# Kernel tuning notes

Measured on AMD Instinct MI355X. Metric: run time of the kernel, lower is better.

The kernel has to match this reference:

```python
import jax, jax.numpy as jnp
import numpy as np

N_NODES = 50000
N_EDGES = 1600000
D_IN = 48
D_OUT = 48


def setup_inputs() -> dict:
    key = jax.random.key(0)
    k1, k2, k3, k4 = jax.random.split(key, 4)
    features = jax.random.normal(k1, (N_NODES, D_IN), dtype=jnp.float32)
    src = jax.random.randint(k2, (N_EDGES,), 0, N_NODES, dtype=jnp.int64)
    dst = jax.random.randint(k3, (N_EDGES,), 0, N_NODES, dtype=jnp.int64)
    # xavier_normal for Linear(48,48): std = sqrt(2/(fan_in+fan_out))
    std = np.sqrt(2.0 / (D_IN + D_OUT))
    W = jax.random.normal(k4, (D_OUT, D_IN), dtype=jnp.float32) * std
    b = jnp.zeros((D_OUT,), dtype=jnp.float32)
    return {"features": features, "src": src, "dst": dst, "W": W, "b": b}


def reference(features, src, dst, W, b):
    n = features.shape[0]
    ones = jnp.ones(src.shape[0], dtype=features.dtype)
    out_deg = jax.ops.segment_sum(ones, src, num_segments=n)
    in_deg = jax.ops.segment_sum(ones, dst, num_segments=n)
    ci = jax.lax.rsqrt(jnp.maximum(out_deg, 1.0))  # per src node
    cj = jax.lax.rsqrt(jnp.maximum(in_deg, 1.0))   # per dst node
    # gather-scale: m_e = h[src_e] * ci[src_e]
    msg = features[src] * ci[src][:, None]          # [E, D_IN]
    # scatter-sum to dst, then scale by cj
    agg = jax.ops.segment_sum(msg, dst, num_segments=n) * cj[:, None]
    # DGL update_all leaves zero-in-degree nodes with their original 'h'
    h = jnp.where(in_deg[:, None] > 0, agg, features)
    out = jax.nn.relu(h @ W.T + b)
    return out
```

## Files before the change

kernel.cpp:

```cpp
#include <hip/hip_runtime.h>

#define N_NODES 50000
#define N_EDGES 1600000
#define D 48

#define EPB 8192
#define PB  196
#define NPB_D 64
#define NBIN_D 782
#define NPB_S 256
#define NBIN_S 196

#define EMAX 3072
#define HS 52

#define RECD_OFF  0
#define SRCB_OFF  6422528
#define CI_OFF    8028160
#define OFFLD_OFF 8228160
#define OFFLS_OFF 8535096

__global__ __launch_bounds__(1024) void k_prep(const int* __restrict__ src,
                                               const int* __restrict__ dst,
                                               unsigned int* __restrict__ rec,
                                               unsigned char* __restrict__ srcb,
                                               unsigned short* __restrict__ offld,
                                               unsigned short* __restrict__ offls) {
    __shared__ int cd[NBIN_D];
    __shared__ int cs[NBIN_S];
    __shared__ int scan[1024];
    __shared__ alignas(16) unsigned int  bufd[EPB];
    __shared__ alignas(16) unsigned char bufs[EPB];
    int tid = threadIdx.x, p = blockIdx.x;
    int base = p * EPB;

    int sv[8], dv[8];
    bool ok[8];
    #pragma unroll
    for (int k = 0; k < 8; ++k) {
        int e = base + tid + k * 1024;
        ok[k] = (e < N_EDGES);
        sv[k] = ok[k] ? src[e] : 0;
        dv[k] = ok[k] ? dst[e] : 0;
    }

    for (int i = tid; i < NBIN_D; i += 1024) cd[i] = 0;
    for (int i = tid; i < NBIN_S; i += 1024) cs[i] = 0;
    __syncthreads();
    #pragma unroll
    for (int k = 0; k < 8; ++k) {
        if (ok[k]) {
            atomicAdd(&cd[dv[k] >> 6], 1);
            atomicAdd(&cs[sv[k] >> 8], 1);
        }
    }
    __syncthreads();

    int own = 0;
    if (tid < NBIN_D) own = cd[tid];
    else if (tid < NBIN_D + NBIN_S) own = cs[tid - NBIN_D];
    scan[tid] = own;
    __syncthreads();
    for (int o = 1; o < 1024; o <<= 1) {
        int x = (tid >= o) ? scan[tid - o] : 0;
        __syncthreads();
        scan[tid] += x;
        __syncthreads();
    }
    int incl = scan[tid];
    int cdt = scan[NBIN_D - 1];
    __syncthreads();

    if (tid < NBIN_D) {
        int ex = incl - own;
        offld[p * (NBIN_D + 1) + tid] = (unsigned short)ex;
        cd[tid] = ex;
        if (tid == NBIN_D - 1) offld[p * (NBIN_D + 1) + NBIN_D] = (unsigned short)incl;
    } else if (tid < NBIN_D + NBIN_S) {
        int t = tid - NBIN_D;
        int ex = (incl - cdt) - own;
        offls[p * (NBIN_S + 1) + t] = (unsigned short)ex;
        cs[t] = ex;
        if (t == NBIN_S - 1) offls[p * (NBIN_S + 1) + NBIN_S] = (unsigned short)(incl - cdt);
    }
    __syncthreads();

    #pragma unroll
    for (int k = 0; k < 8; ++k) {
        if (ok[k]) {
            int s = sv[k], d = dv[k];
            int pd = atomicAdd(&cd[d >> 6], 1);
            bufd[pd] = ((unsigned int)s << 6) | (unsigned int)(d & 63);
            int ps = atomicAdd(&cs[s >> 8], 1);
            bufs[ps] = (unsigned char)s;
        }
    }
    __syncthreads();

    int4* ro = (int4*)(rec + base);
    const int4* bi = (const int4*)bufd;
    for (int i = tid; i < EPB / 4; i += 1024) ro[i] = bi[i];
    unsigned int* so = (unsigned int*)(srcb + base);
    const unsigned int* bs = (const unsigned int*)bufs;
    for (int i = tid; i < EPB / 4; i += 1024) so[i] = bs[i];
}

__global__ __launch_bounds__(512) void k_ci(const unsigned char* __restrict__ srcb,
                                            const unsigned short* __restrict__ offls,
                                            float* __restrict__ ci) {
    __shared__ int cnt[NPB_S];
    int tid = threadIdx.x, sb = blockIdx.x;
    for (int i = tid; i < NPB_S; i += 512) cnt[i] = 0;
    __syncthreads();
    int wave = tid >> 6, lane = tid & 63;
    for (int p = wave; p < PB; p += 8) {
        int beg = offls[p * (NBIN_S + 1) + sb];
        int end = offls[p * (NBIN_S + 1) + sb + 1];
        for (int j = beg + lane; j < end; j += 64)
            atomicAdd(&cnt[srcb[p * EPB + j]], 1);
    }
    __syncthreads();
    int n = sb * NPB_S + tid;
    if (tid < NPB_S && n < N_NODES)
        ci[n] = rsqrtf(fmaxf((float)cnt[tid], 1.0f));
}

__global__ __launch_bounds__(1024, 8) void k_gcn(
    const unsigned int* __restrict__ rec, const unsigned short* __restrict__ offld,
    const float* __restrict__ ci, const float* __restrict__ feat,
    const float* __restrict__ W, const float* __restrict__ b,
    float* __restrict__ out) {
    __shared__ int   craw[EMAX];
    __shared__ int   colb[EMAX];
    __shared__ float hl[NPB_D * HS];
    __shared__ float Wl[D * HS];
    __shared__ float bl[D];
    __shared__ int   ideg[NPB_D];
    __shared__ int   off[NPB_D];
    __shared__ int   cur[NPB_D];
    __shared__ int   runoff[PB + 1];
    __shared__ int   runpos[PB];
    __shared__ int   rs[256];
    int tid = threadIdx.x, bin = blockIdx.x;

    for (int i = tid; i < D * D; i += 1024) Wl[(i / D) * HS + (i % D)] = W[i];
    if (tid < D) bl[tid] = b[tid];
    if (tid < NPB_D) { ideg[tid] = 0; cur[tid] = 0; }

    int rlen = 0;
    if (tid < PB) {
        int o0 = offld[tid * (NBIN_D + 1) + bin];
        int o1 = offld[tid * (NBIN_D + 1) + bin + 1];
        rlen = o1 - o0;
        runpos[tid] = tid * EPB + o0;
    }
    if (tid < 256) rs[tid] = (tid < PB) ? rlen : 0;
    __syncthreads();
    for (int o = 1; o < 256; o <<= 1) {
        int x = 0;
        if (tid < 256 && tid >= o) x = rs[tid - o];
        __syncthreads();
        if (tid < 256) rs[tid] += x;
        __syncthreads();
    }
    if (tid < PB) runoff[tid] = rs[tid] - rlen;
    if (tid == 0) runoff[PB] = rs[PB - 1];
    __syncthreads();
    int cnt = runoff[PB];
    if (cnt > EMAX) cnt = EMAX;

    for (int j = tid; j < cnt; j += 1024) {
        int lo = 0, hi = PB - 1;
        while (lo < hi) {
            int mid = (lo + hi + 1) >> 1;
            if (runoff[mid] <= j) lo = mid; else hi = mid - 1;
        }
        unsigned int r = rec[runpos[lo] + (j - runoff[lo])];
        craw[j] = (int)r;
        atomicAdd(&ideg[r & 63], 1);
    }
    __syncthreads();
    if (tid < NPB_D) {
        int v = ideg[tid];
        int incl = v;
        for (int o = 1; o < 64; o <<= 1) {
            int u = __shfl_up(incl, o);
            if (tid >= o) incl += u;
        }
        off[tid] = incl - v;
    }
    __syncthreads();
    for (int j = tid; j < cnt; j += 1024) {
        int r = craw[j];
        int dl = r & 63;
        int p = atomicAdd(&cur[dl], 1);
        colb[off[dl] + p] = r >> 6;
    }
    __syncthreads();

    int wave = tid >> 6;
    int lane = tid & 63;
    int eslot = lane / 12;
    int d4 = lane - eslot * 12;
    bool lane_ok = (lane < 60);
    const float4* feat4 = (const float4*)feat;

    for (int q = 0; q < 4; ++q) {
        int nl = wave * 4 + q;
        int n = bin * NPB_D + nl;
        int cb = off[nl];
        int deg = ideg[nl];

        float4 acc = make_float4(0.0f, 0.0f, 0.0f, 0.0f);
        for (int c0 = 0; c0 < deg; c0 += 60) {
            int jn = min(60, deg - c0);
            int colv = (lane < jn) ? colb[cb + c0 + lane] : 0;
            float civ = (lane < jn) ? ci[colv] : 0.0f;
            for (int i = 0; i < jn; i += 5) {
                int ei = i + eslot;
                int s = __shfl(colv, ei);
                float c = __shfl(civ, ei);
                if (lane_ok && ei < jn) {
                    float4 f = feat4[(size_t)s * 12 + d4];
                    acc.x = fmaf(f.x, c, acc.x);
                    acc.y = fmaf(f.y, c, acc.y);
                    acc.z = fmaf(f.z, c, acc.z);
                    acc.w = fmaf(f.w, c, acc.w);
                }
            }
        }
        {
            float x1 = __shfl(acc.x, lane + 12), x2 = __shfl(acc.x, lane + 24);
            float x3 = __shfl(acc.x, lane + 36), x4 = __shfl(acc.x, lane + 48);
            float y1 = __shfl(acc.y, lane + 12), y2 = __shfl(acc.y, lane + 24);
            float y3 = __shfl(acc.y, lane + 36), y4 = __shfl(acc.y, lane + 48);
            float z1 = __shfl(acc.z, lane + 12), z2 = __shfl(acc.z, lane + 24);
            float z3 = __shfl(acc.z, lane + 36), z4 = __shfl(acc.z, lane + 48);
            float w1 = __shfl(acc.w, lane + 12), w2 = __shfl(acc.w, lane + 24);
            float w3 = __shfl(acc.w, lane + 36), w4 = __shfl(acc.w, lane + 48);
            acc.x += (x1 + x2) + (x3 + x4);
            acc.y += (y1 + y2) + (y3 + y4);
            acc.z += (z1 + z2) + (z3 + z4);
            acc.w += (w1 + w2) + (w3 + w4);
        }
        if (lane < 12 && n < N_NODES) {
            float4 res;
            if (deg > 0) {
                float cj = rsqrtf((float)deg);
                res = make_float4(acc.x * cj, acc.y * cj, acc.z * cj, acc.w * cj);
            } else {
                res = feat4[(size_t)n * 12 + d4];
            }
            *(float4*)(hl + nl * HS + d4 * 4) = res;
        }
    }
    __syncthreads();

    {
        int nl = tid >> 4;
        int c = tid & 15;
        int n = bin * NPB_D + nl;
        if (n < N_NODES) {
            float a0 = bl[c], a1 = bl[c + 16], a2 = bl[c + 32];
            #pragma unroll
            for (int k4 = 0; k4 < 12; ++k4) {
                float4 hv = *(const float4*)(hl + nl * HS + k4 * 4);
                float4 w0 = *(const float4*)(Wl + c * HS + k4 * 4);
                float4 w1 = *(const float4*)(Wl + (c + 16) * HS + k4 * 4);
                float4 w2 = *(const float4*)(Wl + (c + 32) * HS + k4 * 4);
                a0 = fmaf(hv.x, w0.x, a0); a0 = fmaf(hv.y, w0.y, a0);
                a0 = fmaf(hv.z, w0.z, a0); a0 = fmaf(hv.w, w0.w, a0);
                a1 = fmaf(hv.x, w1.x, a1); a1 = fmaf(hv.y, w1.y, a1);
                a1 = fmaf(hv.z, w1.z, a1); a1 = fmaf(hv.w, w1.w, a1);
                a2 = fmaf(hv.x, w2.x, a2); a2 = fmaf(hv.y, w2.y, a2);
                a2 = fmaf(hv.z, w2.z, a2); a2 = fmaf(hv.w, w2.w, a2);
            }
            float* op = out + (size_t)n * D;
            op[c]      = fmaxf(a0, 0.0f);
            op[c + 16] = fmaxf(a1, 0.0f);
            op[c + 32] = fmaxf(a2, 0.0f);
        }
    }
}

extern "C" void kernel_launch(void* const* d_in, const int* in_sizes, int n_in,
                              void* d_out, int out_size, void* d_ws, size_t ws_size,
                              hipStream_t stream) {
    const float* feat = (const float*)d_in[0];
    const int*   src  = (const int*)d_in[1];
    const int*   dst  = (const int*)d_in[2];
    const float* W    = (const float*)d_in[3];
    const float* b    = (const float*)d_in[4];
    float* out = (float*)d_out;

    char* ws = (char*)d_ws;
    unsigned int*   rec   = (unsigned int*)(ws + RECD_OFF);
    unsigned char*  srcb  = (unsigned char*)(ws + SRCB_OFF);
    float*          ci    = (float*)(ws + CI_OFF);
    unsigned short* offld = (unsigned short*)(ws + OFFLD_OFF);
    unsigned short* offls = (unsigned short*)(ws + OFFLS_OFF);

    k_prep<<<PB, 1024, 0, stream>>>(src, dst, rec, srcb, offld, offls);
    k_ci<<<NBIN_S, 512, 0, stream>>>(srcb, offls, ci);
    k_gcn<<<NBIN_D, 1024, 0, stream>>>(rec, offld, ci, feat, W, b, out);
}
```

Baseline: 159.5 us.

## Fuse three GCN kernels into one persistent kernel with grid barriers

```diff
diff --git a/kernel.cpp b/kernel.cpp
--- a/kernel.cpp
+++ b/kernel.cpp
@@ -4,8 +4,9 @@
 #define N_EDGES 1600000
 #define D 48
 
-#define EPB 8192
-#define PB  196
+#define NB  256
+#define TPB 1024
+#define EPB 6272
 #define NPB_D 64
 #define NBIN_D 782
 #define NPB_S 256
@@ -18,267 +19,315 @@
 #define SRCB_OFF  6422528
 #define CI_OFF    8028160
 #define OFFLD_OFF 8228160
-#define OFFLS_OFF 8535096
-
-__global__ __launch_bounds__(1024) void k_prep(const int* __restrict__ src,
-                                               const int* __restrict__ dst,
-                                               unsigned int* __restrict__ rec,
-                                               unsigned char* __restrict__ srcb,
-                                               unsigned short* __restrict__ offld,
-                                               unsigned short* __restrict__ offls) {
-    __shared__ int cd[NBIN_D];
-    __shared__ int cs[NBIN_S];
-    __shared__ int scan[1024];
-    __shared__ alignas(16) unsigned int  bufd[EPB];
-    __shared__ alignas(16) unsigned char bufs[EPB];
-    int tid = threadIdx.x, p = blockIdx.x;
-    int base = p * EPB;
-
-    int sv[8], dv[8];
-    bool ok[8];
-    #pragma unroll
-    for (int k = 0; k < 8; ++k) {
-        int e = base + tid + k * 1024;
-        ok[k] = (e < N_EDGES);
-        sv[k] = ok[k] ? src[e] : 0;
-        dv[k] = ok[k] ? dst[e] : 0;
-    }
-
-    for (int i = tid; i < NBIN_D; i += 1024) cd[i] = 0;
-    for (int i = tid; i < NBIN_S; i += 1024) cs[i] = 0;
+#define OFFLS_OFF 8629056
+#define BAR_OFF   8729920
+
+__device__ __forceinline__ void gridbar(int* bar, int target) {
     __syncthreads();
-    #pragma unroll
-    for (int k = 0; k < 8; ++k) {
-        if (ok[k]) {
-            atomicAdd(&cd[dv[k] >> 6], 1);
-            atomicAdd(&cs[sv[k] >> 8], 1);
-        }
+    if (threadIdx.x == 0) {
+        __threadfence();
+        atomicAdd(bar, 1);
+        while (atomicAdd(bar, 0) < target)
+            __builtin_amdgcn_s_sleep(4);
+        __threadfence();
     }
     __syncthreads();
-
-    int own = 0;
-    if (tid < NBIN_D) own = cd[tid];
-    else if (tid < NBIN_D + NBIN_S) own = cs[tid - NBIN_D];
-    scan[tid] = own;
-    __syncthreads();
-    for (int o = 1; o < 1024; o <<= 1) {
-        int x = (tid >= o) ? scan[tid - o] : 0;
-        __syncthreads();
-        scan[tid] += x;
-        __syncthreads();
+}
+
+__global__ __launch_bounds__(TPB) void k_fused(
+    const int* __restrict__ src, const int* __restrict__ dst,
+    const float* __restrict__ feat, const float* __restrict__ W,
+    const float* __restrict__ b, float* __restrict__ out,
+    unsigned int* __restrict__ rec, unsigned char* __restrict__ srcb,
+    float* __restrict__ ci, unsigned short* __restrict__ offld,
+    unsigned short* __restrict__ offls, int* bar) {
+
+    __shared__ union U_t {
+        struct {
+            unsigned int bufd[EPB];
+            int scan[TPB];
+            int cd[NBIN_D];
+            int cs[NBIN_S];
+            unsigned char bufs[EPB];
+        } p1;
+        struct { int cnt[NPB_S]; } p2;
+        struct {
+            int   craw[EMAX];
+            int   colb[EMAX];
+            float hl[NPB_D * HS];
+            float Wl[D * HS];
+            float bl[D];
+            int   ideg[NPB_D];
+            int   off[NPB_D];
+            int   cur[NPB_D];
+            int   runpos[NB];
+            int   runoff[NB + 1];
+            int   rs[NB];
+        } p3;
+    } U;
+    static_assert(sizeof(U.p1) < 160 * 1024 && sizeof(U.p3) < 160 * 1024, "lds");
+
+    int tid = threadIdx.x, blk = blockIdx.x;
+
+    {
+        int base = blk * EPB;
+        int sv[7], dv[7];
+        bool ok[7];
+        #pragma unroll
+        for (int k = 0; k < 7; ++k) {
+            int j = tid + k * TPB;
+            int e = base + j;
+            ok[k] = (j < EPB) && (e < N_EDGES);
+            sv[k] = ok[k] ? src[e] : 0;
+            dv[k] = ok[k] ? dst[e] : 0;
+        }
+        for (int i = tid; i < NBIN_D; i += TPB) U.p1.cd[i] = 0;
+        for (int i = tid; i < NBIN_S; i += TPB) U.p1.cs[i] = 0;
+        __syncthreads();
+        #pragma unroll
+        for (int k = 0; k < 7; ++k) {
+            if (ok[k]) {
+                atomicAdd(&U.p1.cd[dv[k] >> 6], 1);
+                atomicAdd(&U.p1.cs[sv[k] >> 8], 1);
+            }
+        }
+        __syncthreads();
+
+        int own = 0;
+        if (tid < NBIN_D) own = U.p1.cd[tid];
+        else if (tid < NBIN_D + NBIN_S) own = U.p1.cs[tid - NBIN_D];
+        U.p1.scan[tid] = own;
+        __syncthreads();
+        for (int o = 1; o < TPB; o <<= 1) {
+            int x = (tid >= o) ? U.p1.scan[tid - o] : 0;
+            __syncthreads();
+            U.p1.scan[tid] += x;
+            __syncthreads();
+        }
+        int incl = U.p1.scan[tid];
+        int cdt = U.p1.scan[NBIN_D - 1];
+        __syncthreads();
+
+        if (tid < NBIN_D) {
+            int ex = incl - own;
+            offld[blk * (NBIN_D + 1) + tid] = (unsigned short)ex;
+            U.p1.cd[tid] = ex;
+            if (tid == NBIN_D - 1) offld[blk * (NBIN_D + 1) + NBIN_D] = (unsigned short)incl;
+        } else if (tid < NBIN_D + NBIN_S) {
+            int t = tid - NBIN_D;
+            int ex = (incl - cdt) - own;
+            offls[blk * (NBIN_S + 1) + t] = (unsigned short)ex;
+            U.p1.cs[t] = ex;
+            if (t == NBIN_S - 1) offls[blk * (NBIN_S + 1) + NBIN_S] = (unsigned short)(incl - cdt);
+        }
+        __syncthreads();
+
+        #pragma unroll
+        for (int k = 0; k < 7; ++k) {
+            if (ok[k]) {
+                int s = sv[k], d = dv[k];
+                int pd = atomicAdd(&U.p1.cd[d >> 6], 1);
+                U.p1.bufd[pd] = ((unsigned int)s << 6) | (unsigned int)(d & 63);
+                int ps = atomicAdd(&U.p1.cs[s >> 8], 1);
+                U.p1.bufs[ps] = (unsigned char)s;
+            }
+        }
+        __syncthreads();
+
+        int4* ro = (int4*)(rec + base);
+        const int4* bi = (const int4*)U.p1.bufd;
+        for (int i = tid; i < EPB / 4; i += TPB) ro[i] = bi[i];
+        unsigned int* so = (unsigned int*)(srcb + base);
+        const unsigned int* bs = (const unsigned int*)U.p1.bufs;
+        for (int i = tid; i < EPB / 4; i += TPB) so[i] = bs[i];
     }
-    int incl = scan[tid];
-    int cdt = scan[NBIN_D - 1];
-    __syncthreads();
-
-    if (tid < NBIN_D) {
-        int ex = incl - own;
-        offld[p * (NBIN_D + 1) + tid] = (unsigned short)ex;
-        cd[tid] = ex;
-        if (tid == NBIN_D - 1) offld[p * (NBIN_D + 1) + NBIN_D] = (unsigned short)incl;
-    } else if (tid < NBIN_D + NBIN_S) {
-        int t = tid - NBIN_D;
-        int ex = (incl - cdt) - own;
-        offls[p * (NBIN_S + 1) + t] = (unsigned short)ex;
-        cs[t] = ex;
-        if (t == NBIN_S - 1) offls[p * (NBIN_S + 1) + NBIN_S] = (unsigned short)(incl - cdt);
+
+    gridbar(bar, NB);
+
+    if (blk < NBIN_S) {
+        int sb = blk;
+        if (tid < NPB_S) U.p2.cnt[tid] = 0;
+        __syncthreads();
+        int wave = tid >> 6, lane = tid & 63;
+        for (int p = wave; p < NB; p += 16) {
+            int o0 = offls[p * (NBIN_S + 1) + sb];
+            int o1 = offls[p * (NBIN_S + 1) + sb + 1];
+            for (int j = o0 + lane; j < o1; j += 64)
+                atomicAdd(&U.p2.cnt[srcb[p * EPB + j]], 1);
+        }
+        __syncthreads();
+        if (tid < NPB_S) {
+            int n = sb * NPB_S + tid;
+            if (n < N_NODES) ci[n] = rsqrtf(fmaxf((float)U.p2.cnt[tid], 1.0f));
+        }
     }
-    __syncthreads();
-
-    #pragma unroll
-    for (int k = 0; k < 8; ++k) {
-        if (ok[k]) {
-            int s = sv[k], d = dv[k];
-            int pd = atomicAdd(&cd[d >> 6], 1);
-            bufd[pd] = ((unsigned int)s << 6) | (unsigned int)(d & 63);
-            int ps = atomicAdd(&cs[s >> 8], 1);
-            bufs[ps] = (unsigned char)s;
-        }
-    }
-    __syncthreads();
-
-    int4* ro = (int4*)(rec + base);
-    const int4* bi = (const int4*)bufd;
-    for (int i = tid; i < EPB / 4; i += 1024) ro[i] = bi[i];
-    unsigned int* so = (unsigned int*)(srcb + base);
-    const unsigned int* bs = (const unsigned int*)bufs;
-    for (int i = tid; i < EPB / 4; i += 1024) so[i] = bs[i];
-}
-
-__global__ __launch_bounds__(512) void k_ci(const unsigned char* __restrict__ srcb,
-                                            const unsigned short* __restrict__ offls,
-                                            float* __restrict__ ci) {
-    __shared__ int cnt[NPB_S];
-    int tid = threadIdx.x, sb = blockIdx.x;
-    for (int i = tid; i < NPB_S; i += 512) cnt[i] = 0;
-    __syncthreads();
+
+    gridbar(bar, 2 * NB);
+
+    for (int i = tid; i < D * D; i += TPB) U.p3.Wl[(i / D) * HS + (i % D)] = W[i];
+    if (tid < D) U.p3.bl[tid] = b[tid];
+
     int wave = tid >> 6, lane = tid & 63;
-    for (int p = wave; p < PB; p += 8) {
-        int beg = offls[p * (NBIN_S + 1) + sb];
-        int end = offls[p * (NBIN_S + 1) + sb + 1];
-        for (int j = beg + lane; j < end; j += 64)
-            atomicAdd(&cnt[srcb[p * EPB + j]], 1);
-    }
-    __syncthreads();
-    int n = sb * NPB_S + tid;
-    if (tid < NPB_S && n < N_NODES)
-        ci[n] = rsqrtf(fmaxf((float)cnt[tid], 1.0f));
-}
-
-__global__ __launch_bounds__(1024, 8) void k_gcn(
-    const unsigned int* __restrict__ rec, const unsigned short* __restrict__ offld,
-    const float* __restrict__ ci, const float* __restrict__ feat,
-    const float* __restrict__ W, const float* __restrict__ b,
-    float* __restrict__ out) {
-    __shared__ int   craw[EMAX];
-    __shared__ int   colb[EMAX];
-    __shared__ float hl[NPB_D * HS];
-    __shared__ float Wl[D * HS];
-    __shared__ float bl[D];
-    __shared__ int   ideg[NPB_D];
-    __shared__ int   off[NPB_D];
-    __shared__ int   cur[NPB_D];
-    __shared__ int   runoff[PB + 1];
-    __shared__ int   runpos[PB];
-    __shared__ int   rs[256];
-    int tid = threadIdx.x, bin = blockIdx.x;
-
-    for (int i = tid; i < D * D; i += 1024) Wl[(i / D) * HS + (i % D)] = W[i];
-    if (tid < D) bl[tid] = b[tid];
-    if (tid < NPB_D) { ideg[tid] = 0; cur[tid] = 0; }
-
-    int rlen = 0;
-    if (tid < PB) {
-        int o0 = offld[tid * (NBIN_D + 1) + bin];
-        int o1 = offld[tid * (NBIN_D + 1) + bin + 1];
-        rlen = o1 - o0;
-        runpos[tid] = tid * EPB + o0;
-    }
-    if (tid < 256) rs[tid] = (tid < PB) ? rlen : 0;
-    __syncthreads();
-    for (int o = 1; o < 256; o <<= 1) {
-        int x = 0;
-        if (tid < 256 && tid >= o) x = rs[tid - o];
-        __syncthreads();
-        if (tid < 256) rs[tid] += x;
-        __syncthreads();
-    }
-    if (tid < PB) runoff[tid] = rs[tid] - rlen;
-    if (tid == 0) runoff[PB] = rs[PB - 1];
-    __syncthreads();
-    int cnt = runoff[PB];
-    if (cnt > EMAX) cnt = EMAX;
-
-    for (int j = tid; j < cnt; j += 1024) {
-        int lo = 0, hi = PB - 1;
-        while (lo < hi) {
-            int mid = (lo + hi + 1) >> 1;
-            if (runoff[mid] <= j) lo = mid; else hi = mid - 1;
-        }
-        unsigned int r = rec[runpos[lo] + (j - runoff[lo])];
-        craw[j] = (int)r;
-        atomicAdd(&ideg[r & 63], 1);
-    }
-    __syncthreads();
-    if (tid < NPB_D) {
-        int v = ideg[tid];
-        int incl = v;
-        for (int o = 1; o < 64; o <<= 1) {
-            int u = __shfl_up(incl, o);
-            if (tid >= o) incl += u;
-        }
-        off[tid] = incl - v;
-    }
-    __syncthreads();
-    for (int j = tid; j < cnt; j += 1024) {
-        int r = craw[j];
-        int dl = r & 63;
-        int p = atomicAdd(&cur[dl], 1);
-        colb[off[dl] + p] = r >> 6;
-    }
-    __syncthreads();
-
-    int wave = tid >> 6;
-    int lane = tid & 63;
     int eslot = lane / 12;
     int d4 = lane - eslot * 12;
     bool lane_ok = (lane < 60);
     const float4* feat4 = (const float4*)feat;
 
-    for (int q = 0; q < 4; ++q) {
-        int nl = wave * 4 + q;
-        int n = bin * NPB_D + nl;
-        int cb = off[nl];
-        int deg = ideg[nl];
-
-        float4 acc = make_float4(0.0f, 0.0f, 0.0f, 0.0f);
-        for (int c0 = 0; c0 < deg; c0 += 60) {
-            int jn = min(60, deg - c0);
-            int colv = (lane < jn) ? colb[cb + c0 + lane] : 0;
-            float civ = (lane < jn) ? ci[colv] : 0.0f;
-            for (int i = 0; i < jn; i += 5) {
+    for (int bin = blk; bin < NBIN_D; bin += NB) {
+        __syncthreads();
+        if (tid < NPB_D) { U.p3.ideg[tid] = 0; U.p3.cur[tid] = 0; }
+        int rl = 0;
+        if (tid < NB) {
+            int o0 = offld[tid * (NBIN_D + 1) + bin];
+            int o1 = offld[tid * (NBIN_D + 1) + bin + 1];
+            rl = o1 - o0;
+            U.p3.runpos[tid] = tid * EPB + o0;
+            U.p3.rs[tid] = rl;
+        }
+        __syncthreads();
+        for (int o = 1; o < NB; o <<= 1) {
+            int x = 0;
+            if (tid < NB && tid >= o) x = U.p3.rs[tid - o];
+            __syncthreads();
+            if (tid < NB) U.p3.rs[tid] += x;
+            __syncthreads();
+        }
+        if (tid < NB) U.p3.runoff[tid] = U.p3.rs[tid] - rl;
+        if (tid == 0) U.p3.runoff[NB] = U.p3.rs[NB - 1];
+        __syncthreads();
+
+        {
+            int r = tid >> 2, sub = tid & 3;
+            int rbase = U.p3.runoff[r];
+            int rlen = U.p3.runoff[r + 1] - rbase;
+            int gpos = U.p3.runpos[r];
+            for (int j = sub; j < rlen; j += 4) {
+                int idx = rbase + j;
+                if (idx < EMAX) {
+                    int v = (int)rec[gpos + j];
+                    U.p3.craw[idx] = v;
+                    atomicAdd(&U.p3.ideg[v & 63], 1);
+                }
+            }
+        }
+        __syncthreads();
+        int cnt = U.p3.runoff[NB];
+        if (cnt > EMAX) cnt = EMAX;
+
+        if (tid < NPB_D) {
+            int v = U.p3.ideg[tid];
+            int incl = v;
+            for (int o = 1; o < 64; o <<= 1) {
+                int u = __shfl_up(incl, o);
+                if (tid >= o) incl += u;
+            }
+            U.p3.off[tid] = incl - v;
+        }
+        __syncthreads();
+        for (int j = tid; j < cnt; j += TPB) {
+            int r = U.p3.craw[j];
+            int dl = r & 63;
+            int p = atomicAdd(&U.p3.cur[dl], 1);
+            U.p3.colb[U.p3.off[dl] + p] = r >> 6;
+        }
+        __syncthreads();
+
+        int nl0 = wave * 4;
+        int degq[4], cbq[4];
+        float4 acc[4];
+        #pragma unroll
+        for (int q = 0; q < 4; ++q) {
+            degq[q] = U.p3.ideg[nl0 + q];
+            cbq[q] = U.p3.off[nl0 + q];
+            acc[q] = make_float4(0.0f, 0.0f, 0.0f, 0.0f);
+        }
+        int maxdeg = max(max(degq[0], degq[1]), max(degq[2], degq[3]));
+        for (int c0 = 0; c0 < maxdeg; c0 += 60) {
+            int colv[4]; float civ[4]; int jnq[4];
+            #pragma unroll
+            for (int q = 0; q < 4; ++q) {
+                int jn = degq[q] - c0;
+                jnq[q] = jn < 60 ? jn : 60;
+                colv[q] = (lane < jnq[q]) ? U.p3.colb[cbq[q] + c0 + lane] : 0;
+                civ[q]  = (lane < jnq[q]) ? ci[colv[q]] : 0.0f;
+            }
+            int rem = maxdeg - c0;
+            int maxjn = rem < 60 ? rem : 60;
+            for (int i = 0; i < maxjn; i += 5) {
                 int ei = i + eslot;
-                int s = __shfl(colv, ei);
-                float c = __shfl(civ, ei);
-                if (lane_ok && ei < jn) {
-                    float4 f = feat4[(size_t)s * 12 + d4];
-                    acc.x = fmaf(f.x, c, acc.x);
-                    acc.y = fmaf(f.y, c, acc.y);
-                    acc.z = fmaf(f.z, c, acc.z);
-                    acc.w = fmaf(f.w, c, acc.w);
-                }
-            }
-        }
+                int sq[4]; float cq[4];
+                #pragma unroll
+                for (int q = 0; q < 4; ++q) {
+                    sq[q] = __shfl(colv[q], ei);
+                    cq[q] = __shfl(civ[q], ei);
+                }
+                #pragma unroll
+                for (int q = 0; q < 4; ++q) {
+                    if (lane_ok && ei < jnq[q]) {
+                        float4 f = feat4[(size_t)sq[q] * 12 + d4];
+                        acc[q].x = fmaf(f.x, cq[q], acc[q].x);
+                        acc[q].y = fmaf(f.y, cq[q], acc[q].y);
+                        acc[q].z = fmaf(f.z, cq[q], acc[q].z);
+                        acc[q].w = fmaf(f.w, cq[q], acc[q].w);
+                    }
+                }
+            }
+        }
+        #pragma unroll
+        for (int q = 0; q < 4; ++q) {
+            float4 a = acc[q];
+            float x1 = __shfl(a.x, lane + 12), x2 = __shfl(a.x, lane + 24);
+            float x3 = __shfl(a.x, lane + 36), x4 = __shfl(a.x, lane + 48);
+            float y1 = __shfl(a.y, lane + 12), y2 = __shfl(a.y, lane + 24);
+            float y3 = __shfl(a.y, lane + 36), y4 = __shfl(a.y, lane + 48);
+            float z1 = __shfl(a.z, lane + 12), z2 = __shfl(a.z, lane + 24);
+            float z3 = __shfl(a.z, lane + 36), z4 = __shfl(a.z, lane + 48);
+            float w1 = __shfl(a.w, lane + 12), w2 = __shfl(a.w, lane + 24);
+            float w3 = __shfl(a.w, lane + 36), w4 = __shfl(a.w, lane + 48);
+            a.x += (x1 + x2) + (x3 + x4);
+            a.y += (y1 + y2) + (y3 + y4);
+            a.z += (z1 + z2) + (z3 + z4);
+            a.w += (w1 + w2) + (w3 + w4);
+            int nl = nl0 + q;
+            int n = bin * NPB_D + nl;
+            if (lane < 12 && n < N_NODES) {
+                float4 res;
+                int deg = degq[q];
+                if (deg > 0) {
+                    float cj = rsqrtf((float)deg);
+                    res = make_float4(a.x * cj, a.y * cj, a.z * cj, a.w * cj);
+                } else {
+                    res = feat4[(size_t)n * 12 + d4];
+                }
+                *(float4*)(U.p3.hl + nl * HS + d4 * 4) = res;
+            }
+        }
+        __syncthreads();
+
         {
-            float x1 = __shfl(acc.x, lane + 12), x2 = __shfl(acc.x, lane + 24);
-            float x3 = __shfl(acc.x, lane + 36), x4 = __shfl(acc.x, lane + 48);
-            float y1 = __shfl(acc.y, lane + 12), y2 = __shfl(acc.y, lane + 24);
-            float y3 = __shfl(acc.y, lane + 36), y4 = __shfl(acc.y, lane + 48);
-            float z1 = __shfl(acc.z, lane + 12), z2 = __shfl(acc.z, lane + 24);
-            float z3 = __shfl(acc.z, lane + 36), z4 = __shfl(acc.z, lane + 48);
-            float w1 = __shfl(acc.w, lane + 12), w2 = __shfl(acc.w, lane + 24);
-            float w3 = __shfl(acc.w, lane + 36), w4 = __shfl(acc.w, lane + 48);
-            acc.x += (x1 + x2) + (x3 + x4);
-            acc.y += (y1 + y2) + (y3 + y4);
-            acc.z += (z1 + z2) + (z3 + z4);
-            acc.w += (w1 + w2) + (w3 + w4);
-        }
-        if (lane < 12 && n < N_NODES) {
-            float4 res;
-            if (deg > 0) {
-                float cj = rsqrtf((float)deg);
-                res = make_float4(acc.x * cj, acc.y * cj, acc.z * cj, acc.w * cj);
-            } else {
-                res = feat4[(size_t)n * 12 + d4];
-            }
-            *(float4*)(hl + nl * HS + d4 * 4) = res;
-        }
-    }
-    __syncthreads();
-
-    {
-        int nl = tid >> 4;
-        int c = tid & 15;
-        int n = bin * NPB_D + nl;
-        if (n < N_NODES) {
-            float a0 = bl[c], a1 = bl[c + 16], a2 = bl[c + 32];
-            #pragma unroll
-            for (int k4 = 0; k4 < 12; ++k4) {
-                float4 hv = *(const float4*)(hl + nl * HS + k4 * 4);
-                float4 w0 = *(const float4*)(Wl + c * HS + k4 * 4);
-                float4 w1 = *(const float4*)(Wl + (c + 16) * HS + k4 * 4);
-                float4 w2 = *(const float4*)(Wl + (c + 32) * HS + k4 * 4);
-                a0 = fmaf(hv.x, w0.x, a0); a0 = fmaf(hv.y, w0.y, a0);
-                a0 = fmaf(hv.z, w0.z, a0); a0 = fmaf(hv.w, w0.w, a0);
-                a1 = fmaf(hv.x, w1.x, a1); a1 = fmaf(hv.y, w1.y, a1);
-                a1 = fmaf(hv.z, w1.z, a1); a1 = fmaf(hv.w, w1.w, a1);
-                a2 = fmaf(hv.x, w2.x, a2); a2 = fmaf(hv.y, w2.y, a2);
-                a2 = fmaf(hv.z, w2.z, a2); a2 = fmaf(hv.w, w2.w, a2);
-            }
-            float* op = out + (size_t)n * D;
-            op[c]      = fmaxf(a0, 0.0f);
-            op[c + 16] = fmaxf(a1, 0.0f);
-            op[c + 32] = fmaxf(a2, 0.0f);
+            int nl = tid >> 4;
+            int c = tid & 15;
+            int n = bin * NPB_D + nl;
+            if (n < N_NODES) {
+                float a0 = U.p3.bl[c], a1 = U.p3.bl[c + 16], a2 = U.p3.bl[c + 32];
+                #pragma unroll
+                for (int k4 = 0; k4 < 12; ++k4) {
+                    float4 hv = *(const float4*)(U.p3.hl + nl * HS + k4 * 4);
+                    float4 w0 = *(const float4*)(U.p3.Wl + c * HS + k4 * 4);
+                    float4 w1 = *(const float4*)(U.p3.Wl + (c + 16) * HS + k4 * 4);
+                    float4 w2 = *(const float4*)(U.p3.Wl + (c + 32) * HS + k4 * 4);
+                    a0 = fmaf(hv.x, w0.x, a0); a0 = fmaf(hv.y, w0.y, a0);
+                    a0 = fmaf(hv.z, w0.z, a0); a0 = fmaf(hv.w, w0.w, a0);
+                    a1 = fmaf(hv.x, w1.x, a1); a1 = fmaf(hv.y, w1.y, a1);
+                    a1 = fmaf(hv.z, w1.z, a1); a1 = fmaf(hv.w, w1.w, a1);
+                    a2 = fmaf(hv.x, w2.x, a2); a2 = fmaf(hv.y, w2.y, a2);
+                    a2 = fmaf(hv.z, w2.z, a2); a2 = fmaf(hv.w, w2.w, a2);
+                }
+                float* op = out + (size_t)n * D;
+                op[c]      = fmaxf(a0, 0.0f);
+                op[c + 16] = fmaxf(a1, 0.0f);
+                op[c + 32] = fmaxf(a2, 0.0f);
+            }
         }
     }
 }
@@ -299,8 +348,9 @@
     float*          ci    = (float*)(ws + CI_OFF);
     unsigned short* offld = (unsigned short*)(ws + OFFLD_OFF);
     unsigned short* offls = (unsigned short*)(ws + OFFLS_OFF);
-
-    k_prep<<<PB, 1024, 0, stream>>>(src, dst, rec, srcb, offld, offls);
-    k_ci<<<NBIN_S, 512, 0, stream>>>(srcb, offls, ci);
-    k_gcn<<<NBIN_D, 1024, 0, stream>>>(rec, offld, ci, feat, W, b, out);
+    int*            bar   = (int*)(ws + BAR_OFF);
+
+    hipMemsetAsync(bar, 0, 8, stream);
+    k_fused<<<NB, TPB, 0, stream>>>(src, dst, feat, W, b, out,
+                                    rec, srcb, ci, offld, offls, bar);
 }
```

Measured after the change: 237.0 us. 48.6% more time.

## Prescale features by ci in k_ci, use wave-shuffle scans, halve gcn block size

Applied to the files above, without the earlier changes.

```diff
diff --git a/kernel.cpp b/kernel.cpp
--- a/kernel.cpp
+++ b/kernel.cpp
@@ -16,9 +16,11 @@
 
 #define RECD_OFF  0
 #define SRCB_OFF  6422528
-#define CI_OFF    8028160
-#define OFFLD_OFF 8228160
-#define OFFLS_OFF 8535096
+#define OFFLD_OFF 8028160
+#define OFFLS_OFF 8335104
+#define CI_OFF    8412416
+#define SFEAT_OFF 8612416
+#define SFEAT_END 18212416
 
 __global__ __launch_bounds__(1024) void k_prep(const int* __restrict__ src,
                                                const int* __restrict__ dst,
@@ -28,10 +30,12 @@
                                                unsigned short* __restrict__ offls) {
     __shared__ int cd[NBIN_D];
     __shared__ int cs[NBIN_S];
-    __shared__ int scan[1024];
+    __shared__ int wsum[16], wexcl[16];
+    __shared__ int cdt_s;
     __shared__ alignas(16) unsigned int  bufd[EPB];
     __shared__ alignas(16) unsigned char bufs[EPB];
     int tid = threadIdx.x, p = blockIdx.x;
+    int wave = tid >> 6, lane = tid & 63;
     int base = p * EPB;
 
     int sv[8], dv[8];
@@ -59,29 +63,41 @@
     int own = 0;
     if (tid < NBIN_D) own = cd[tid];
     else if (tid < NBIN_D + NBIN_S) own = cs[tid - NBIN_D];
-    scan[tid] = own;
-    __syncthreads();
-    for (int o = 1; o < 1024; o <<= 1) {
-        int x = (tid >= o) ? scan[tid - o] : 0;
-        __syncthreads();
-        scan[tid] += x;
-        __syncthreads();
-    }
-    int incl = scan[tid];
-    int cdt = scan[NBIN_D - 1];
-    __syncthreads();
+    int incl = own;
+    #pragma unroll
+    for (int o = 1; o < 64; o <<= 1) {
+        int u = __shfl_up(incl, o);
+        if (lane >= o) incl += u;
+    }
+    if (lane == 63) wsum[wave] = incl;
+    __syncthreads();
+    if (tid < 16) {
+        int v = wsum[tid];
+        int ic = v;
+        #pragma unroll
+        for (int o = 1; o < 16; o <<= 1) {
+            int u = __shfl_up(ic, o);
+            if (lane >= o) ic += u;
+        }
+        wexcl[tid] = ic - v;
+    }
+    __syncthreads();
+    int gincl = wexcl[wave] + incl;
+    if (tid == NBIN_D - 1) cdt_s = gincl;
+    __syncthreads();
+    int cdt = cdt_s;
 
     if (tid < NBIN_D) {
-        int ex = incl - own;
+        int ex = gincl - own;
         offld[p * (NBIN_D + 1) + tid] = (unsigned short)ex;
         cd[tid] = ex;
-        if (tid == NBIN_D - 1) offld[p * (NBIN_D + 1) + NBIN_D] = (unsigned short)incl;
+        if (tid == NBIN_D - 1) offld[p * (NBIN_D + 1) + NBIN_D] = (unsigned short)gincl;
     } else if (tid < NBIN_D + NBIN_S) {
         int t = tid - NBIN_D;
-        int ex = (incl - cdt) - own;
+        int ex = (gincl - cdt) - own;
         offls[p * (NBIN_S + 1) + t] = (unsigned short)ex;
         cs[t] = ex;
-        if (t == NBIN_S - 1) offls[p * (NBIN_S + 1) + NBIN_S] = (unsigned short)(incl - cdt);
+        if (t == NBIN_S - 1) offls[p * (NBIN_S + 1) + NBIN_S] = (unsigned short)(gincl - cdt);
     }
     __syncthreads();
 
@@ -107,8 +123,12 @@
 
 __global__ __launch_bounds__(512) void k_ci(const unsigned char* __restrict__ srcb,
                                             const unsigned short* __restrict__ offls,
-                                            float* __restrict__ ci) {
+                                            const float* __restrict__ feat,
+                                            float* __restrict__ ci,
+                                            float* __restrict__ sfeat,
+                                            int do_scale) {
     __shared__ int cnt[NPB_S];
+    __shared__ float cl[NPB_S];
     int tid = threadIdx.x, sb = blockIdx.x;
     for (int i = tid; i < NPB_S; i += 512) cnt[i] = 0;
     __syncthreads();
@@ -120,17 +140,33 @@
             atomicAdd(&cnt[srcb[p * EPB + j]], 1);
     }
     __syncthreads();
-    int n = sb * NPB_S + tid;
-    if (tid < NPB_S && n < N_NODES)
-        ci[n] = rsqrtf(fmaxf((float)cnt[tid], 1.0f));
+    if (tid < NPB_S) {
+        float c = rsqrtf(fmaxf((float)cnt[tid], 1.0f));
+        cl[tid] = c;
+        int n = sb * NPB_S + tid;
+        if (n < N_NODES) ci[n] = c;
+    }
+    __syncthreads();
+    if (do_scale) {
+        int nb = sb * NPB_S;
+        int lim4 = (min(NPB_S, N_NODES - nb)) * 12;
+        const float4* f4 = (const float4*)feat + (size_t)nb * 12;
+        float4* s4 = (float4*)sfeat + (size_t)nb * 12;
+        for (int i = tid; i < lim4; i += 512) {
+            float sc = cl[i / 12];
+            float4 f = f4[i];
+            s4[i] = make_float4(f.x * sc, f.y * sc, f.z * sc, f.w * sc);
+        }
+    }
 }
 
-__global__ __launch_bounds__(1024, 8) void k_gcn(
+template <bool PRESCALED>
+__global__ __launch_bounds__(512, 8) void k_gcn(
     const unsigned int* __restrict__ rec, const unsigned short* __restrict__ offld,
-    const float* __restrict__ ci, const float* __restrict__ feat,
+    const float* __restrict__ ci, const float* __restrict__ sfeat,
+    const float* __restrict__ feat,
     const float* __restrict__ W, const float* __restrict__ b,
     float* __restrict__ out) {
-    __shared__ int   craw[EMAX];
     __shared__ int   colb[EMAX];
     __shared__ float hl[NPB_D * HS];
     __shared__ float Wl[D * HS];
@@ -140,10 +176,11 @@
     __shared__ int   cur[NPB_D];
     __shared__ int   runoff[PB + 1];
     __shared__ int   runpos[PB];
-    __shared__ int   rs[256];
+    __shared__ int   wsum[8], wexcl[8];
     int tid = threadIdx.x, bin = blockIdx.x;
-
-    for (int i = tid; i < D * D; i += 1024) Wl[(i / D) * HS + (i % D)] = W[i];
+    int wave = tid >> 6, lane = tid & 63;
+
+    for (int i = tid; i < D * D; i += 512) Wl[(i / D) * HS + (i % D)] = W[i];
     if (tid < D) bl[tid] = b[tid];
     if (tid < NPB_D) { ideg[tid] = 0; cur[tid] = 0; }
 
@@ -154,59 +191,77 @@
         rlen = o1 - o0;
         runpos[tid] = tid * EPB + o0;
     }
-    if (tid < 256) rs[tid] = (tid < PB) ? rlen : 0;
-    __syncthreads();
-    for (int o = 1; o < 256; o <<= 1) {
-        int x = 0;
-        if (tid < 256 && tid >= o) x = rs[tid - o];
-        __syncthreads();
-        if (tid < 256) rs[tid] += x;
-        __syncthreads();
-    }
-    if (tid < PB) runoff[tid] = rs[tid] - rlen;
-    if (tid == 0) runoff[PB] = rs[PB - 1];
+    int incl = rlen;
+    #pragma unroll
+    for (int o = 1; o < 64; o <<= 1) {
+        int u = __shfl_up(incl, o);
+        if (lane >= o) incl += u;
+    }
+    if (lane == 63) wsum[wave] = incl;
+    __syncthreads();
+    if (tid < 8) {
+        int v = wsum[tid];
+        int ic = v;
+        #pragma unroll
+        for (int o = 1; o < 8; o <<= 1) {
+            int u = __shfl_up(ic, o);
+            if (lane >= o) ic += u;
+        }
+        wexcl[tid] = ic - v;
+        if (tid == 7) runoff[PB] = ic;
+    }
+    __syncthreads();
+    if (tid < PB) runoff[tid] = wexcl[wave] + incl - rlen;
     __syncthreads();
     int cnt = runoff[PB];
     if (cnt > EMAX) cnt = EMAX;
 
-    for (int j = tid; j < cnt; j += 1024) {
-        int lo = 0, hi = PB - 1;
-        while (lo < hi) {
-            int mid = (lo + hi + 1) >> 1;
-            if (runoff[mid] <= j) lo = mid; else hi = mid - 1;
-        }
-        unsigned int r = rec[runpos[lo] + (j - runoff[lo])];
-        craw[j] = (int)r;
-        atomicAdd(&ideg[r & 63], 1);
+    unsigned int rr[6];
+    #pragma unroll
+    for (int k = 0; k < 6; ++k) {
+        int j = tid + k * 512;
+        rr[k] = 0xFFFFFFFFu;
+        if (j < cnt) {
+            int lo = 0, hi = PB - 1;
+            while (lo < hi) {
+                int mid = (lo + hi + 1) >> 1;
+                if (runoff[mid] <= j) lo = mid; else hi = mid - 1;
+            }
+            unsigned int r = rec[runpos[lo] + (j - runoff[lo])];
+            rr[k] = r;
+            atomicAdd(&ideg[r & 63], 1);
+        }
     }
     __syncthreads();
     if (tid < NPB_D) {
         int v = ideg[tid];
-        int incl = v;
+        int ic = v;
+        #pragma unroll
         for (int o = 1; o < 64; o <<= 1) {
-            int u = __shfl_up(incl, o);
-            if (tid >= o) incl += u;
-        }
-        off[tid] = incl - v;
-    }
-    __syncthreads();
-    for (int j = tid; j < cnt; j += 1024) {
-        int r = craw[j];
-        int dl = r & 63;
-        int p = atomicAdd(&cur[dl], 1);
-        colb[off[dl] + p] = r >> 6;
-    }
-    __syncthreads();
-
-    int wave = tid >> 6;
-    int lane = tid & 63;
+            int u = __shfl_up(ic, o);
+            if (tid >= o) ic += u;
+        }
+        off[tid] = ic - v;
+    }
+    __syncthreads();
+    #pragma unroll
+    for (int k = 0; k < 6; ++k) {
+        if (rr[k] != 0xFFFFFFFFu) {
+            int dl = rr[k] & 63;
+            int p = atomicAdd(&cur[dl], 1);
+            colb[off[dl] + p] = (int)(rr[k] >> 6);
+        }
+    }
+    __syncthreads();
+
     int eslot = lane / 12;
     int d4 = lane - eslot * 12;
     bool lane_ok = (lane < 60);
     const float4* feat4 = (const float4*)feat;
-
-    for (int q = 0; q < 4; ++q) {
-        int nl = wave * 4 + q;
+    const float4* sf4 = (const float4*)sfeat;
+
+    for (int q = 0; q < 8; ++q) {
+        int nl = wave * 8 + q;
         int n = bin * NPB_D + nl;
         int cb = off[nl];
         int deg = ideg[nl];
@@ -215,17 +270,23 @@
         for (int c0 = 0; c0 < deg; c0 += 60) {
             int jn = min(60, deg - c0);
             int colv = (lane < jn) ? colb[cb + c0 + lane] : 0;
-            float civ = (lane < jn) ? ci[colv] : 0.0f;
+            float civ = 0.0f;
+            if (!PRESCALED) civ = (lane < jn) ? ci[colv] : 0.0f;
             for (int i = 0; i < jn; i += 5) {
                 int ei = i + eslot;
                 int s = __shfl(colv, ei);
-                float c = __shfl(civ, ei);
+                float c = PRESCALED ? 0.0f : __shfl(civ, ei);
                 if (lane_ok && ei < jn) {
-                    float4 f = feat4[(size_t)s * 12 + d4];
-                    acc.x = fmaf(f.x, c, acc.x);
-                    acc.y = fmaf(f.y, c, acc.y);
-                    acc.z = fmaf(f.z, c, acc.z);
-                    acc.w = fmaf(f.w, c, acc.w);
+                    if (PRESCALED) {
+                        float4 f = sf4[(size_t)s * 12 + d4];
+                        acc.x += f.x; acc.y += f.y; acc.z += f.z; acc.w += f.w;
+                    } else {
+                        float4 f = feat4[(size_t)s * 12 + d4];
+                        acc.x = fmaf(f.x, c, acc.x);
+                        acc.y = fmaf(f.y, c, acc.y);
+                        acc.z = fmaf(f.z, c, acc.z);
+                        acc.w = fmaf(f.w, c, acc.w);
+                    }
                 }
             }
         }
@@ -256,8 +317,9 @@
     }
     __syncthreads();
 
-    {
-        int nl = tid >> 4;
+    #pragma unroll
+    for (int half = 0; half < 2; ++half) {
+        int nl = (tid >> 4) + half * 32;
         int c = tid & 15;
         int n = bin * NPB_D + nl;
         if (n < N_NODES) {
@@ -296,11 +358,17 @@
     char* ws = (char*)d_ws;
     unsigned int*   rec   = (unsigned int*)(ws + RECD_OFF);
     unsigned char*  srcb  = (unsigned char*)(ws + SRCB_OFF);
-    float*          ci    = (float*)(ws + CI_OFF);
     unsigned short* offld = (unsigned short*)(ws + OFFLD_OFF);
     unsigned short* offls = (unsigned short*)(ws + OFFLS_OFF);
+    float*          ci    = (float*)(ws + CI_OFF);
+    float*          sfeat = (float*)(ws + SFEAT_OFF);
+
+    const bool prescale = (ws_size >= (size_t)SFEAT_END);
 
     k_prep<<<PB, 1024, 0, stream>>>(src, dst, rec, srcb, offld, offls);
-    k_ci<<<NBIN_S, 512, 0, stream>>>(srcb, offls, ci);
-    k_gcn<<<NBIN_D, 1024, 0, stream>>>(rec, offld, ci, feat, W, b, out);
+    k_ci<<<NBIN_S, 512, 0, stream>>>(srcb, offls, feat, ci, sfeat, prescale ? 1 : 0);
+    if (prescale)
+        k_gcn<true><<<NBIN_D, 512, 0, stream>>>(rec, offld, ci, sfeat, feat, W, b, out);
+    else
+        k_gcn<false><<<NBIN_D, 512, 0, stream>>>(rec, offld, ci, sfeat, feat, W, b, out);
 }
```

After: 147.6 us. 7.5% less time.
